# Kernel optimization log

Hardware: AMD Instinct MI355X
Metric: run time of the kernel (lower is better)

The kernel has to match this reference:

```python
import jax, jax.numpy as jnp
import numpy as np

C = 1.0
TAU = 1.0
LE = 1.0
LH = 1.0
LN_EPS = 1e-5

def _safe_norm(x, keepdims=False):
    return jnp.clip(jnp.sqrt(jnp.sum(x * x, axis=-1, keepdims=keepdims)), 1e-15)

def _project_to_ball(x, c, eps=1e-5):
    sqrt_c = c ** 0.5
    norm = _safe_norm(x, keepdims=True)
    max_norm = (1.0 - eps) / sqrt_c
    scale = jnp.where(norm > max_norm, max_norm / norm, 1.0)
    return x * scale

def _lambda_x(x, c):
    x = _project_to_ball(x, c)
    x2 = jnp.sum(x * x, axis=-1, keepdims=True)
    return 2.0 / jnp.clip(1.0 - c * x2, 1e-15)

def _mobius_add(x, y, c):
    x = _project_to_ball(x, c)
    y = _project_to_ball(y, c)
    x2 = jnp.sum(x * x, axis=-1, keepdims=True)
    y2 = jnp.sum(y * y, axis=-1, keepdims=True)
    xy = jnp.sum(x * y, axis=-1, keepdims=True)
    num = (1 + 2 * c * xy + c * y2) * x + (1 - c * x2) * y
    den = 1 + 2 * c * xy + c ** 2 * x2 * y2
    return num / jnp.clip(den, 1e-15)

def _exp_map_x(x, v, c):
    sqrt_c = c ** 0.5
    lam = _lambda_x(x, c)
    vnorm = _safe_norm(v, keepdims=True)
    v_dir = v / vnorm
    factor = jnp.tanh(lam * sqrt_c * vnorm / 2.0) / sqrt_c
    out = _mobius_add(x, v_dir * factor, c)
    return _project_to_ball(out, c)

def _log_map_x(x, y, c):
    sqrt_c = c ** 0.5
    lam = _lambda_x(x, c)
    u = _mobius_add(-x, y, c)
    unorm = _safe_norm(u, keepdims=True)
    u_dir = u / unorm
    arg = jnp.minimum(sqrt_c * unorm, 1 - 1e-7)
    scale = 2.0 / (lam * sqrt_c) * jnp.arctanh(arg)
    return scale * u_dir

def _poincare_distance_sq(x, y, c):
    sqrt_c = c ** 0.5
    x = _project_to_ball(x, c)
    y = _project_to_ball(y, c)
    diff = _mobius_add(-x, y, c)
    norm = _safe_norm(diff, keepdims=False)
    arg = jnp.minimum(sqrt_c * norm, 1 - 1e-7)
    dist = 2.0 / sqrt_c * jnp.arctanh(arg)
    return dist * dist

def setup_inputs() -> dict:
    key = jax.random.key(0)
    ks = jax.random.split(key, 6)
    B, N, L, A, de, dh, z_dim = 8, 8, 64, 64, 128, 64, 128
    z_e, z_h = z_dim // 2 + z_dim % 2, z_dim // 2
    return {
        "curr_rho_batch": jax.random.normal(ks[0], (B, A, de), jnp.float32),
        "curr_hyp_emb": 0.1 * jax.random.normal(ks[1], (B, dh), jnp.float32),
        "demo_rho_batch": jax.random.normal(ks[2], (B, N, L, A, de), jnp.float32),
        "demo_hyp_emb": 0.1 * jax.random.normal(ks[3], (B, N, L, dh), jnp.float32),
        "We": 0.02 * jax.random.normal(ks[4], (z_e, de), jnp.float32),
        "Wh": 0.02 * jax.random.normal(ks[5], (z_h, dh), jnp.float32),
        "ln_gamma": jnp.ones((z_dim,), jnp.float32),
        "ln_beta": jnp.zeros((z_dim,), jnp.float32),
    }

def reference(curr_rho_batch, curr_hyp_emb, demo_rho_batch, demo_hyp_emb, We, Wh, ln_gamma, ln_beta):
    B, A, de = curr_rho_batch.shape
    _, N, L, _, _ = demo_rho_batch.shape
    M = N * L
    dh = curr_hyp_emb.shape[-1]
    demo_rho_flat = demo_rho_batch.reshape(B, M, A, de)   # [B,M,A,de]
    demo_hyp_flat = demo_hyp_emb.reshape(B, M, dh)        # [B,M,dh]
    # Euclidean squared distances: [B,M,A] -> [B,A,M]
    e_diff_sq = jnp.sum((curr_rho_batch[:, None, :, :] - demo_rho_flat) ** 2, axis=-1)
    e_diff_sq = jnp.transpose(e_diff_sq, (0, 2, 1))
    # Hyperbolic squared distances: [B,M]
    dH2 = _poincare_distance_sq(curr_hyp_emb[:, None, :], demo_hyp_flat, C)
    scores = -(LH * dH2[:, None, :] + LE * e_diff_sq) / max(TAU, 1e-8)  # [B,A,M]
    alpha = jax.nn.softmax(scores, axis=-1)
    # Euclidean aggregation
    e_out = jnp.einsum('bam,bmad->bad', alpha, demo_rho_flat)  # [B,A,de]
    # Hyperbolic Karcher-mean step
    log_vecs = _log_map_x(curr_hyp_emb[:, None, :], demo_hyp_flat, C)  # [B,M,dh]
    v = jnp.einsum('bam,bmd->bad', alpha, log_vecs)  # [B,A,dh]
    x_ba = jnp.broadcast_to(curr_hyp_emb[:, None, :], (B, A, dh))
    h_out = _exp_map_x(x_ba, v, C)  # [B,A,dh]
    z = jnp.concatenate([e_out @ We.T, h_out @ Wh.T], axis=-1)  # [B,A,z_dim]
    mean = jnp.mean(z, axis=-1, keepdims=True)
    var = jnp.var(z, axis=-1, keepdims=True)
    z = (z - mean) / jnp.sqrt(var + LN_EPS) * ln_gamma + ln_beta
    return z
```

## Files before the change

### kernel.cpp

```cpp
#include <hip/hip_runtime.h>

#define DEV __device__ __forceinline__

constexpr int A_ = 64, DE = 128, M_ = 512, DH = 64;

DEV float wred_sum64(float v) {
#pragma unroll
    for (int o = 1; o < 64; o <<= 1) v += __shfl_xor(v, o, 64);
    return v;
}

__global__ __launch_bounds__(256) void k_hyp(const float* __restrict__ curr_hyp,
                                             const float* __restrict__ demo_hyp,
                                             float* __restrict__ dH2,
                                             float* __restrict__ logv) {
    const int lane = threadIdx.x & 63;
    const int r    = (blockIdx.x << 2) + (threadIdx.x >> 6);
    const int b    = r >> 9;

    float x = curr_hyp[(b << 6) + lane];
    float y = demo_hyp[((size_t)r << 6) + lane];
    const float mx = 1.0f - 1e-5f;

    float x2r = wred_sum64(x * x);
    float xn  = fmaxf(sqrtf(x2r), 1e-15f);
    float sx  = xn > mx ? mx / xn : 1.0f;
    x *= sx;
    float x2 = x2r * sx * sx;
    float y2r = wred_sum64(y * y);
    float yn  = fmaxf(sqrtf(y2r), 1e-15f);
    float sy  = yn > mx ? mx / yn : 1.0f;
    y *= sy;
    float y2 = y2r * sy * sy;

    float xy = wred_sum64(x * y);
    float num = (1.f - 2.f * xy + y2) * (-x) + (1.f - x2) * y;
    float den = fmaxf(1.f - 2.f * xy + x2 * y2, 1e-15f);
    float u   = num / den;

    float u2  = wred_sum64(u * u);
    float un  = fmaxf(sqrtf(u2), 1e-15f);
    float arg = fminf(un, 1.f - 1e-7f);
    float at  = 0.5f * __logf((1.f + arg) / (1.f - arg));

    if (lane == 0) dH2[r] = 4.f * at * at;

    float lamden = fmaxf(1.f - x2, 1e-15f);
    float ls     = lamden * at / un;
    logv[((size_t)r << 6) + lane] = ls * u;
}

__global__ __launch_bounds__(512, 4) void k_main(const float* __restrict__ curr_rho,
                                                 const float* __restrict__ demo_rho,
                                                 const float* __restrict__ curr_hyp,
                                                 const float* __restrict__ dH2,
                                                 const float* __restrict__ logv,
                                                 const float* __restrict__ We,
                                                 const float* __restrict__ Wh,
                                                 const float* __restrict__ gamma,
                                                 const float* __restrict__ beta,
                                                 float* __restrict__ out) {
    __shared__ __align__(16) float rede[32 * 132];
    __shared__ float lds_sc[512];
    __shared__ float lds_dh[512];
    __shared__ float redm[8];
    __shared__ float reds[8];
    __shared__ float vpart[8][64];
    __shared__ float eh[192];

    const int t    = threadIdx.x;
    const int lane = t & 63;
    const int wv   = t >> 6;
    const int dp   = t & 15;
    const int mi   = t >> 4;
    const int blk  = blockIdx.x;
    const int b    = blk >> 6, a = blk & 63;

    lds_dh[t] = dH2[(b << 9) + t];

    float qf[8];
    {
        float4 q0 = *(const float4*)(curr_rho + (size_t)blk * DE + dp * 8);
        float4 q1 = *(const float4*)(curr_rho + (size_t)blk * DE + dp * 8 + 4);
        qf[0] = q0.x; qf[1] = q0.y; qf[2] = q0.z; qf[3] = q0.w;
        qf[4] = q1.x; qf[5] = q1.y; qf[6] = q1.z; qf[7] = q1.w;
    }

    const size_t rowStride = (size_t)A_ * DE;
    const size_t cstep     = (size_t)32 * rowStride;
    const float* tp = demo_rho + ((size_t)b * M_ * A_ + a) * DE + (size_t)mi * rowStride + dp * 8;

    __syncthreads();

    float4 ka0 = *(const float4*)tp;
    float4 ka1 = *(const float4*)(tp + 4);
    float4 kb0 = *(const float4*)(tp + cstep);
    float4 kb1 = *(const float4*)(tp + cstep + 4);

    float e_acc[8];
#pragma unroll
    for (int j = 0; j < 8; j++) e_acc[j] = 0.f;
    float gmax = -1e30f, gsum = 0.f;

#pragma unroll 2
    for (int c = 0; c < 16; ++c) {
        float4 n0, n1;
        if (c + 2 < 16) {
            const float* np = tp + (size_t)(c + 2) * cstep;
            n0 = *(const float4*)np;
            n1 = *(const float4*)(np + 4);
        }
        float kf[8];
        kf[0] = ka0.x; kf[1] = ka0.y; kf[2] = ka0.z; kf[3] = ka0.w;
        kf[4] = ka1.x; kf[5] = ka1.y; kf[6] = ka1.z; kf[7] = ka1.w;

        float ps = 0.f;
#pragma unroll
        for (int j = 0; j < 8; j++) { float d = qf[j] - kf[j]; ps += d * d; }
        ps += __shfl_xor(ps, 1, 64);
        ps += __shfl_xor(ps, 2, 64);
        ps += __shfl_xor(ps, 4, 64);
        ps += __shfl_xor(ps, 8, 64);
        float sc = -(lds_dh[c * 32 + mi] + ps);
        if (dp == 0) lds_sc[c * 32 + mi] = sc;

        float lm = fmaxf(sc, __shfl_xor(sc, 16, 64));
        lm = fmaxf(lm, __shfl_xor(lm, 32, 64));
        float gnew = fmaxf(gmax, lm);
        float r1   = __expf(gmax - gnew);
        float wexp = __expf(sc - gnew);
        float wsum = wexp + __shfl_xor(wexp, 16, 64);
        wsum += __shfl_xor(wsum, 32, 64);
        gsum = fmaf(gsum, r1, wsum);
#pragma unroll
        for (int j = 0; j < 8; j++) e_acc[j] = fmaf(wexp, kf[j], e_acc[j] * r1);
        gmax = gnew;

        ka0 = kb0; ka1 = kb1; kb0 = n0; kb1 = n1;
    }

    if (lane == 0) { redm[wv] = gmax; reds[wv] = gsum; }
    __syncthreads();

    float M = redm[0];
#pragma unroll
    for (int w = 1; w < 8; w++) M = fmaxf(M, redm[w]);
    float S = 0.f;
#pragma unroll
    for (int w = 0; w < 8; w++) S += reds[w] * __expf(redm[w] - M);
    const float inv = 1.f / S;
    const float fw  = __expf(gmax - M);

    float al = __expf(lds_sc[t] - M) * inv;

    *(float4*)&rede[mi * 132 + dp * 8] =
        make_float4(e_acc[0] * fw, e_acc[1] * fw, e_acc[2] * fw, e_acc[3] * fw);
    *(float4*)&rede[mi * 132 + dp * 8 + 4] =
        make_float4(e_acc[4] * fw, e_acc[5] * fw, e_acc[6] * fw, e_acc[7] * fw);
    lds_sc[t] = al;
    __syncthreads();

    if (t < 128) {
        float s = 0.f;
#pragma unroll
        for (int g = 0; g < 32; g++) s += rede[g * 132 + t];
        eh[t] = s * inv;
    }

    {
        const float* lvb = logv + ((size_t)(b * M_) + wv * 64) * DH;
        float acc = 0.f;
#pragma unroll 8
        for (int i = 0; i < 64; ++i)
            acc = fmaf(lds_sc[wv * 64 + i], lvb[(size_t)i * DH + lane], acc);
        vpart[wv][lane] = acc;
    }
    __syncthreads();

    if (wv == 0) {
        float v = 0.f;
#pragma unroll
        for (int w = 0; w < 8; w++) v += vpart[w][lane];

        const float mx = 1.0f - 1e-5f;
        float x = curr_hyp[(b << 6) + lane];
        float x2r = wred_sum64(x * x);
        float xn  = fmaxf(sqrtf(x2r), 1e-15f);
        float sx  = xn > mx ? mx / xn : 1.f;
        x *= sx;
        float x2 = x2r * sx * sx;
        float lamden = fmaxf(1.f - x2, 1e-15f);

        float v2 = wred_sum64(v * v);
        float vn = fmaxf(sqrtf(v2), 1e-15f);
        float targ   = vn / lamden;
        float e2     = __expf(2.f * targ);
        float factor = 1.f - 2.f / (e2 + 1.f);
        float wvv    = v * (factor / vn);

        float w2 = wred_sum64(wvv * wvv);
        float xw = wred_sum64(x * wvv);
        float num = (1.f + 2.f * xw + w2) * x + (1.f - x2) * wvv;
        float den = fmaxf(1.f + 2.f * xw + x2 * w2, 1e-15f);
        float h   = num / den;
        float h2  = wred_sum64(h * h);
        float hn  = fmaxf(sqrtf(h2), 1e-15f);
        float shh = hn > mx ? mx / hn : 1.f;
        h *= shh;
        eh[128 + lane] = h;

        float ze = 0.f;
        const float* werow = We + lane * 128;
#pragma unroll
        for (int d0 = 0; d0 < 128; d0 += 4) {
            float4 wv4 = *(const float4*)(werow + d0);
            ze = fmaf(eh[d0 + 0], wv4.x, ze);
            ze = fmaf(eh[d0 + 1], wv4.y, ze);
            ze = fmaf(eh[d0 + 2], wv4.z, ze);
            ze = fmaf(eh[d0 + 3], wv4.w, ze);
        }
        float zh = 0.f;
        const float* whrow = Wh + lane * 64;
#pragma unroll
        for (int d0 = 0; d0 < 64; d0 += 4) {
            float4 wv4 = *(const float4*)(whrow + d0);
            zh = fmaf(eh[128 + d0 + 0], wv4.x, zh);
            zh = fmaf(eh[128 + d0 + 1], wv4.y, zh);
            zh = fmaf(eh[128 + d0 + 2], wv4.z, zh);
            zh = fmaf(eh[128 + d0 + 3], wv4.w, zh);
        }
        float ssum = wred_sum64(ze + zh);
        float mean = ssum * (1.f / 128.f);
        float sq   = wred_sum64(ze * ze + zh * zh);
        float var  = sq * (1.f / 128.f) - mean * mean;
        float rinv = rsqrtf(var + 1e-5f);
        float oe = (ze - mean) * rinv * gamma[lane] + beta[lane];
        float oh = (zh - mean) * rinv * gamma[64 + lane] + beta[64 + lane];
        out[(size_t)blk * 128 + lane]      = oe;
        out[(size_t)blk * 128 + 64 + lane] = oh;
    }
}

extern "C" void kernel_launch(void* const* d_in, const int* in_sizes, int n_in,
                              void* d_out, int out_size, void* d_ws, size_t ws_size,
                              hipStream_t stream) {
    const float* curr_rho = (const float*)d_in[0];
    const float* curr_hyp = (const float*)d_in[1];
    const float* demo_rho = (const float*)d_in[2];
    const float* demo_hyp = (const float*)d_in[3];
    const float* We       = (const float*)d_in[4];
    const float* Wh       = (const float*)d_in[5];
    const float* gamma    = (const float*)d_in[6];
    const float* beta     = (const float*)d_in[7];
    float* out = (float*)d_out;

    float* ws   = (float*)d_ws;
    float* dH2  = ws;
    float* logv = ws + 4096;

    k_hyp<<<1024, 256, 0, stream>>>(curr_hyp, demo_hyp, dH2, logv);
    k_main<<<512, 512, 0, stream>>>(curr_rho, demo_rho, curr_hyp, dH2, logv,
                                    We, Wh, gamma, beta, out);
}
```

Baseline: 209.9 us.

## Split main kernel into split-M online-softmax stream pass and combine kernel

Replaces the single per-(b,a) main kernel with a flash-decoding style split: k_stream processes 16-row chunks of M per block with an online softmax, streaming demo_rho with register prefetch, and writes partial max/sum/accumulators and raw scores to workspace. k_comb merges the 32 partials per (b,a), recomputes the hyperbolic weighted sum from the stored scores, and applies the exp map, projections and layernorm. The aim is to read the large demo_rho tensor with better parallelism and coalescing. The cost is an extra launch and several MB of workspace traffic. The old kernel is kept as a fallback when the workspace is too small.

```diff
diff --git a/kernel.cpp b/kernel.cpp
--- a/kernel.cpp
+++ b/kernel.cpp
@@ -50,16 +50,237 @@
     logv[((size_t)r << 6) + lane] = ls * u;
 }
 
-__global__ __launch_bounds__(512, 4) void k_main(const float* __restrict__ curr_rho,
+__global__ __launch_bounds__(1024) void k_stream(const float* __restrict__ curr_rho,
                                                  const float* __restrict__ demo_rho,
-                                                 const float* __restrict__ curr_hyp,
                                                  const float* __restrict__ dH2,
-                                                 const float* __restrict__ logv,
-                                                 const float* __restrict__ We,
-                                                 const float* __restrict__ Wh,
-                                                 const float* __restrict__ gamma,
-                                                 const float* __restrict__ beta,
-                                                 float* __restrict__ out) {
+                                                 float* __restrict__ ws_m,
+                                                 float* __restrict__ ws_s,
+                                                 float* __restrict__ ws_e,
+                                                 float* __restrict__ ws_sc) {
+    const int t   = threadIdx.x;
+    const int mi  = t >> 4;
+    const int dp  = t & 15;
+    const int blk = blockIdx.x;
+    const int b   = blk >> 5, mc = blk & 31;
+    const int m0  = mc << 4;
+
+    float qf[8];
+    {
+        const float* qp = curr_rho + ((size_t)(b * 64 + mi)) * DE + dp * 8;
+        float4 q0 = *(const float4*)qp;
+        float4 q1 = *(const float4*)(qp + 4);
+        qf[0] = q0.x; qf[1] = q0.y; qf[2] = q0.z; qf[3] = q0.w;
+        qf[4] = q1.x; qf[5] = q1.y; qf[6] = q1.z; qf[7] = q1.w;
+    }
+
+    float dh2r[16];
+    {
+        const float* dp2 = dH2 + (b << 9) + m0;
+        *(float4*)&dh2r[0]  = *(const float4*)(dp2);
+        *(float4*)&dh2r[4]  = *(const float4*)(dp2 + 4);
+        *(float4*)&dh2r[8]  = *(const float4*)(dp2 + 8);
+        *(float4*)&dh2r[12] = *(const float4*)(dp2 + 12);
+    }
+
+    const float* tp = demo_rho + ((size_t)(b * M_ + m0)) * (A_ * DE) + mi * DE + dp * 8;
+
+    float4 pa0 = *(const float4*)tp;
+    float4 pa1 = *(const float4*)(tp + 4);
+    float4 pb0 = *(const float4*)(tp + 8192);
+    float4 pb1 = *(const float4*)(tp + 8192 + 4);
+    float4 pc0 = *(const float4*)(tp + 16384);
+    float4 pc1 = *(const float4*)(tp + 16384 + 4);
+
+    float e_acc[8];
+#pragma unroll
+    for (int j = 0; j < 8; j++) e_acc[j] = 0.f;
+    float gmax = -1e30f, gsum = 0.f;
+
+    float* scp = ws_sc + ((size_t)blk * 16) * 64;
+
+#pragma unroll
+    for (int c = 0; c < 16; ++c) {
+        float4 n0 = make_float4(0.f, 0.f, 0.f, 0.f);
+        float4 n1 = n0;
+        if (c + 3 < 16) {
+            const float* np = tp + (size_t)(c + 3) * 8192;
+            n0 = *(const float4*)np;
+            n1 = *(const float4*)(np + 4);
+        }
+        float kf[8];
+        kf[0] = pa0.x; kf[1] = pa0.y; kf[2] = pa0.z; kf[3] = pa0.w;
+        kf[4] = pa1.x; kf[5] = pa1.y; kf[6] = pa1.z; kf[7] = pa1.w;
+
+        float ps = 0.f;
+#pragma unroll
+        for (int j = 0; j < 8; j++) { float d = qf[j] - kf[j]; ps += d * d; }
+        ps += __shfl_xor(ps, 1, 64);
+        ps += __shfl_xor(ps, 2, 64);
+        ps += __shfl_xor(ps, 4, 64);
+        ps += __shfl_xor(ps, 8, 64);
+
+        float sc = -(dh2r[c] + ps);
+        if (dp == 0) scp[c * 64 + mi] = sc;
+
+        float gnew = fmaxf(gmax, sc);
+        float r1   = __expf(gmax - gnew);
+        float w    = __expf(sc - gnew);
+        gsum = fmaf(gsum, r1, w);
+#pragma unroll
+        for (int j = 0; j < 8; j++) e_acc[j] = fmaf(w, kf[j], e_acc[j] * r1);
+        gmax = gnew;
+
+        pa0 = pb0; pa1 = pb1; pb0 = pc0; pb1 = pc1; pc0 = n0; pc1 = n1;
+    }
+
+    float* ep = ws_e + ((size_t)(blk * 64 + mi)) * 128 + dp * 8;
+    *(float4*)ep       = make_float4(e_acc[0], e_acc[1], e_acc[2], e_acc[3]);
+    *(float4*)(ep + 4) = make_float4(e_acc[4], e_acc[5], e_acc[6], e_acc[7]);
+    if (dp == 0) {
+        ws_m[blk * 64 + mi] = gmax;
+        ws_s[blk * 64 + mi] = gsum;
+    }
+}
+
+__global__ __launch_bounds__(256) void k_comb(const float* __restrict__ curr_hyp,
+                                              const float* __restrict__ logv,
+                                              const float* __restrict__ ws_m,
+                                              const float* __restrict__ ws_s,
+                                              const float* __restrict__ ws_e,
+                                              const float* __restrict__ ws_sc,
+                                              const float* __restrict__ We,
+                                              const float* __restrict__ Wh,
+                                              const float* __restrict__ gamma,
+                                              const float* __restrict__ beta,
+                                              float* __restrict__ out) {
+    __shared__ float facL[32];
+    __shared__ float sMS[2];
+    __shared__ float ehL[192];
+    __shared__ float vpart[4][64];
+
+    const int t   = threadIdx.x;
+    const int blk = blockIdx.x;
+    const int b   = blk >> 6, a = blk & 63;
+
+    float g = -1e30f, s = 0.f;
+    if (t < 32) {
+        g = ws_m[(size_t)(b * 32 + t) * 64 + a];
+        s = ws_s[(size_t)(b * 32 + t) * 64 + a];
+    }
+    float M = g;
+    M = fmaxf(M, __shfl_xor(M, 1, 64));
+    M = fmaxf(M, __shfl_xor(M, 2, 64));
+    M = fmaxf(M, __shfl_xor(M, 4, 64));
+    M = fmaxf(M, __shfl_xor(M, 8, 64));
+    M = fmaxf(M, __shfl_xor(M, 16, 64));
+    float fac = __expf(g - M);
+    float Sp  = s * fac;
+    Sp += __shfl_xor(Sp, 1, 64);
+    Sp += __shfl_xor(Sp, 2, 64);
+    Sp += __shfl_xor(Sp, 4, 64);
+    Sp += __shfl_xor(Sp, 8, 64);
+    Sp += __shfl_xor(Sp, 16, 64);
+    if (t < 32) facL[t] = fac;
+    if (t == 0) { sMS[0] = M; sMS[1] = Sp; }
+    __syncthreads();
+    const float Mg   = sMS[0];
+    const float invS = 1.f / sMS[1];
+
+    if (t < 128) {
+        float acc = 0.f;
+#pragma unroll
+        for (int mc = 0; mc < 32; ++mc)
+            acc = fmaf(ws_e[((size_t)((b * 32 + mc) * 64 + a)) * 128 + t], facL[mc], acc);
+        ehL[t] = acc * invS;
+    }
+
+    {
+        const int dh = t & 63, sg = t >> 6;
+        const float* lvb = logv  + ((size_t)(b * M_ + sg * 128)) * 64 + dh;
+        const float* scb = ws_sc + ((size_t)(b * M_ + sg * 128)) * 64 + a;
+        float vac = 0.f;
+#pragma unroll 8
+        for (int i = 0; i < 128; ++i) {
+            float w = __expf(scb[(size_t)i * 64] - Mg);
+            vac = fmaf(w, lvb[(size_t)i * 64], vac);
+        }
+        vpart[sg][dh] = vac;
+    }
+    __syncthreads();
+
+    if (t < 64) {
+        const int lane = t;
+        float v = (vpart[0][lane] + vpart[1][lane] + vpart[2][lane] + vpart[3][lane]) * invS;
+
+        const float mx = 1.0f - 1e-5f;
+        float x = curr_hyp[(b << 6) + lane];
+        float x2r = wred_sum64(x * x);
+        float xn  = fmaxf(sqrtf(x2r), 1e-15f);
+        float sx  = xn > mx ? mx / xn : 1.f;
+        x *= sx;
+        float x2 = x2r * sx * sx;
+        float lamden = fmaxf(1.f - x2, 1e-15f);
+
+        float v2 = wred_sum64(v * v);
+        float vn = fmaxf(sqrtf(v2), 1e-15f);
+        float targ   = vn / lamden;
+        float e2     = __expf(2.f * targ);
+        float factor = 1.f - 2.f / (e2 + 1.f);
+        float wvv    = v * (factor / vn);
+
+        float w2 = wred_sum64(wvv * wvv);
+        float xw = wred_sum64(x * wvv);
+        float num = (1.f + 2.f * xw + w2) * x + (1.f - x2) * wvv;
+        float den = fmaxf(1.f + 2.f * xw + x2 * w2, 1e-15f);
+        float h   = num / den;
+        float h2  = wred_sum64(h * h);
+        float hn  = fmaxf(sqrtf(h2), 1e-15f);
+        float shh = hn > mx ? mx / hn : 1.f;
+        h *= shh;
+        ehL[128 + lane] = h;
+
+        float ze = 0.f;
+        const float* werow = We + lane * 128;
+#pragma unroll
+        for (int d0 = 0; d0 < 128; d0 += 4) {
+            float4 wv4 = *(const float4*)(werow + d0);
+            ze = fmaf(ehL[d0 + 0], wv4.x, ze);
+            ze = fmaf(ehL[d0 + 1], wv4.y, ze);
+            ze = fmaf(ehL[d0 + 2], wv4.z, ze);
+            ze = fmaf(ehL[d0 + 3], wv4.w, ze);
+        }
+        float zh = 0.f;
+        const float* whrow = Wh + lane * 64;
+#pragma unroll
+        for (int d0 = 0; d0 < 64; d0 += 4) {
+            float4 wv4 = *(const float4*)(whrow + d0);
+            zh = fmaf(ehL[128 + d0 + 0], wv4.x, zh);
+            zh = fmaf(ehL[128 + d0 + 1], wv4.y, zh);
+            zh = fmaf(ehL[128 + d0 + 2], wv4.z, zh);
+            zh = fmaf(ehL[128 + d0 + 3], wv4.w, zh);
+        }
+        float ssum = wred_sum64(ze + zh);
+        float mean = ssum * (1.f / 128.f);
+        float sq   = wred_sum64(ze * ze + zh * zh);
+        float var  = sq * (1.f / 128.f) - mean * mean;
+        float rinv = rsqrtf(var + 1e-5f);
+        float oe = (ze - mean) * rinv * gamma[lane] + beta[lane];
+        float oh = (zh - mean) * rinv * gamma[64 + lane] + beta[64 + lane];
+        out[(size_t)blk * 128 + lane]      = oe;
+        out[(size_t)blk * 128 + 64 + lane] = oh;
+    }
+}
+
+__global__ __launch_bounds__(512, 4) void k_main_fb(const float* __restrict__ curr_rho,
+                                                    const float* __restrict__ demo_rho,
+                                                    const float* __restrict__ curr_hyp,
+                                                    const float* __restrict__ dH2,
+                                                    const float* __restrict__ logv,
+                                                    const float* __restrict__ We,
+                                                    const float* __restrict__ Wh,
+                                                    const float* __restrict__ gamma,
+                                                    const float* __restrict__ beta,
+                                                    float* __restrict__ out) {
     __shared__ __align__(16) float rede[32 * 132];
     __shared__ float lds_sc[512];
     __shared__ float lds_dh[512];
@@ -259,6 +480,18 @@
     float* logv = ws + 4096;
 
     k_hyp<<<1024, 256, 0, stream>>>(curr_hyp, demo_hyp, dH2, logv);
-    k_main<<<512, 512, 0, stream>>>(curr_rho, demo_rho, curr_hyp, dH2, logv,
-                                    We, Wh, gamma, beta, out);
-}
+
+    const size_t NEED = (size_t)2658304 * sizeof(float);
+    if (ws_size >= NEED) {
+        float* ws_m  = ws + 266240;
+        float* ws_s  = ws + 282624;
+        float* ws_e  = ws + 299008;
+        float* ws_sc = ws + 2396160;
+        k_stream<<<256, 1024, 0, stream>>>(curr_rho, demo_rho, dH2, ws_m, ws_s, ws_e, ws_sc);
+        k_comb<<<512, 256, 0, stream>>>(curr_hyp, logv, ws_m, ws_s, ws_e, ws_sc,
+                                        We, Wh, gamma, beta, out);
+    } else {
+        k_main_fb<<<512, 512, 0, stream>>>(curr_rho, demo_rho, curr_hyp, dH2, logv,
+                                           We, Wh, gamma, beta, out);
+    }
+}
```

After: 240.4 us. +14.5%, slower.

## Split attention into split-M streaming kernel and separate combine kernel

Applied to the files above, without the earlier changes.

Restructures the main kernel so each block covers 4 agents over a quarter of the demo slots. Each wave reads contiguous 2KB rows of demo_rho instead of strided 512B rows, and prefetch depth goes from 2 to 3. Partial max, sum, weighted e-sums and raw scores are written to the workspace. A new combine kernel merges the four partials, recomputes the softmax weights from the stored scores, and runs the hyperbolic aggregation, exp map, projection and layernorm. This adds one kernel launch and extra global traffic for scores and partials in exchange for better coalescing of the dominant demo_rho stream.

```diff
diff --git a/kernel.cpp b/kernel.cpp
--- a/kernel.cpp
+++ b/kernel.cpp
@@ -50,69 +50,72 @@
     logv[((size_t)r << 6) + lane] = ls * u;
 }
 
-__global__ __launch_bounds__(512, 4) void k_main(const float* __restrict__ curr_rho,
-                                                 const float* __restrict__ demo_rho,
-                                                 const float* __restrict__ curr_hyp,
-                                                 const float* __restrict__ dH2,
-                                                 const float* __restrict__ logv,
-                                                 const float* __restrict__ We,
-                                                 const float* __restrict__ Wh,
-                                                 const float* __restrict__ gamma,
-                                                 const float* __restrict__ beta,
-                                                 float* __restrict__ out) {
-    __shared__ __align__(16) float rede[32 * 132];
-    __shared__ float lds_sc[512];
-    __shared__ float lds_dh[512];
-    __shared__ float redm[8];
-    __shared__ float reds[8];
-    __shared__ float vpart[8][64];
-    __shared__ float eh[192];
-
-    const int t    = threadIdx.x;
-    const int lane = t & 63;
-    const int wv   = t >> 6;
-    const int dp   = t & 15;
-    const int mi   = t >> 4;
-    const int blk  = blockIdx.x;
-    const int b    = blk >> 6, a = blk & 63;
-
-    lds_dh[t] = dH2[(b << 9) + t];
+__global__ __launch_bounds__(512, 4) void k_stream2(const float* __restrict__ curr_rho,
+                                                    const float* __restrict__ demo_rho,
+                                                    const float* __restrict__ dH2,
+                                                    float* __restrict__ ws_m,
+                                                    float* __restrict__ ws_s,
+                                                    float* __restrict__ ws_e,
+                                                    float* __restrict__ ws_sc) {
+    __shared__ float lds_dh[128];
+    __shared__ float redm[8][4];
+    __shared__ float reds[8][4];
+    __shared__ __align__(16) float rede[8][512];
+
+    const int t  = threadIdx.x;
+    const int l  = t & 63;
+    const int mi = t >> 6;
+    const int al = l >> 4;
+    const int dp = l & 15;
+    const int blk = blockIdx.x;
+    const int b  = blk >> 6;
+    const int rr = blk & 63;
+    const int mq = rr >> 4;
+    const int aq = rr & 15;
+    const int a  = aq * 4 + al;
+    const int m0 = mq << 7;
+
+    if (t < 128) lds_dh[t] = dH2[(b << 9) + m0 + t];
 
     float qf[8];
     {
-        float4 q0 = *(const float4*)(curr_rho + (size_t)blk * DE + dp * 8);
-        float4 q1 = *(const float4*)(curr_rho + (size_t)blk * DE + dp * 8 + 4);
+        const float* qp = curr_rho + ((size_t)(b * 64 + a)) * DE + dp * 8;
+        float4 q0 = *(const float4*)qp;
+        float4 q1 = *(const float4*)(qp + 4);
         qf[0] = q0.x; qf[1] = q0.y; qf[2] = q0.z; qf[3] = q0.w;
         qf[4] = q1.x; qf[5] = q1.y; qf[6] = q1.z; qf[7] = q1.w;
     }
 
-    const size_t rowStride = (size_t)A_ * DE;
-    const size_t cstep     = (size_t)32 * rowStride;
-    const float* tp = demo_rho + ((size_t)b * M_ * A_ + a) * DE + (size_t)mi * rowStride + dp * 8;
+    const float* tp = demo_rho + ((size_t)(b * M_ + m0)) * (A_ * DE)
+                    + (size_t)mi * 8192 + aq * 4 * DE + al * DE + dp * 8;
+    const size_t CS = 65536;
 
     __syncthreads();
 
-    float4 ka0 = *(const float4*)tp;
-    float4 ka1 = *(const float4*)(tp + 4);
-    float4 kb0 = *(const float4*)(tp + cstep);
-    float4 kb1 = *(const float4*)(tp + cstep + 4);
+    float4 pa0 = *(const float4*)tp;
+    float4 pa1 = *(const float4*)(tp + 4);
+    float4 pb0 = *(const float4*)(tp + CS);
+    float4 pb1 = *(const float4*)(tp + CS + 4);
+    float4 pc0 = *(const float4*)(tp + 2 * CS);
+    float4 pc1 = *(const float4*)(tp + 2 * CS + 4);
 
     float e_acc[8];
 #pragma unroll
     for (int j = 0; j < 8; j++) e_acc[j] = 0.f;
     float gmax = -1e30f, gsum = 0.f;
 
-#pragma unroll 2
+#pragma unroll 4
     for (int c = 0; c < 16; ++c) {
-        float4 n0, n1;
-        if (c + 2 < 16) {
-            const float* np = tp + (size_t)(c + 2) * cstep;
+        float4 n0 = make_float4(0.f, 0.f, 0.f, 0.f);
+        float4 n1 = n0;
+        if (c + 3 < 16) {
+            const float* np = tp + (size_t)(c + 3) * CS;
             n0 = *(const float4*)np;
             n1 = *(const float4*)(np + 4);
         }
         float kf[8];
-        kf[0] = ka0.x; kf[1] = ka0.y; kf[2] = ka0.z; kf[3] = ka0.w;
-        kf[4] = ka1.x; kf[5] = ka1.y; kf[6] = ka1.z; kf[7] = ka1.w;
+        kf[0] = pa0.x; kf[1] = pa0.y; kf[2] = pa0.z; kf[3] = pa0.w;
+        kf[4] = pa1.x; kf[5] = pa1.y; kf[6] = pa1.z; kf[7] = pa1.w;
 
         float ps = 0.f;
 #pragma unroll
@@ -121,66 +124,108 @@
         ps += __shfl_xor(ps, 2, 64);
         ps += __shfl_xor(ps, 4, 64);
         ps += __shfl_xor(ps, 8, 64);
-        float sc = -(lds_dh[c * 32 + mi] + ps);
-        if (dp == 0) lds_sc[c * 32 + mi] = sc;
-
-        float lm = fmaxf(sc, __shfl_xor(sc, 16, 64));
-        lm = fmaxf(lm, __shfl_xor(lm, 32, 64));
-        float gnew = fmaxf(gmax, lm);
+
+        float sc = -(lds_dh[c * 8 + mi] + ps);
+        if (dp == 0)
+            ws_sc[((size_t)(b * M_ + m0 + c * 8 + mi)) * 64 + a] = sc;
+
+        float gnew = fmaxf(gmax, sc);
         float r1   = __expf(gmax - gnew);
-        float wexp = __expf(sc - gnew);
-        float wsum = wexp + __shfl_xor(wexp, 16, 64);
-        wsum += __shfl_xor(wsum, 32, 64);
-        gsum = fmaf(gsum, r1, wsum);
-#pragma unroll
-        for (int j = 0; j < 8; j++) e_acc[j] = fmaf(wexp, kf[j], e_acc[j] * r1);
+        float w    = __expf(sc - gnew);
+        gsum = fmaf(gsum, r1, w);
+#pragma unroll
+        for (int j = 0; j < 8; j++) e_acc[j] = fmaf(w, kf[j], e_acc[j] * r1);
         gmax = gnew;
 
-        ka0 = kb0; ka1 = kb1; kb0 = n0; kb1 = n1;
-    }
-
-    if (lane == 0) { redm[wv] = gmax; reds[wv] = gsum; }
+        pa0 = pb0; pa1 = pb1; pb0 = pc0; pb1 = pc1; pc0 = n0; pc1 = n1;
+    }
+
+    if (dp == 0) { redm[mi][al] = gmax; reds[mi][al] = gsum; }
     __syncthreads();
 
-    float M = redm[0];
-#pragma unroll
-    for (int w = 1; w < 8; w++) M = fmaxf(M, redm[w]);
+    float Mb = redm[0][al];
+#pragma unroll
+    for (int k = 1; k < 8; k++) Mb = fmaxf(Mb, redm[k][al]);
+    float Sb = 0.f;
+#pragma unroll
+    for (int k = 0; k < 8; k++) Sb += reds[k][al] * __expf(redm[k][al] - Mb);
+    float fac = __expf(gmax - Mb);
+
+    *(float4*)&rede[mi][al * 128 + dp * 8] =
+        make_float4(e_acc[0] * fac, e_acc[1] * fac, e_acc[2] * fac, e_acc[3] * fac);
+    *(float4*)&rede[mi][al * 128 + dp * 8 + 4] =
+        make_float4(e_acc[4] * fac, e_acc[5] * fac, e_acc[6] * fac, e_acc[7] * fac);
+    if (mi == 0 && dp == 0) {
+        const int q = b * 4 + mq;
+        ws_m[q * 64 + a] = Mb;
+        ws_s[q * 64 + a] = Sb;
+    }
+    __syncthreads();
+
+    {
+        const int al2 = t >> 7, dd = t & 127;
+        float s = 0.f;
+#pragma unroll
+        for (int k = 0; k < 8; k++) s += rede[k][al2 * 128 + dd];
+        ws_e[((size_t)(b * 4 + mq) * 64 + (aq * 4 + al2)) * 128 + dd] = s;
+    }
+}
+
+__global__ __launch_bounds__(256) void k_comb2(const float* __restrict__ curr_hyp,
+                                               const float* __restrict__ logv,
+                                               const float* __restrict__ ws_m,
+                                               const float* __restrict__ ws_s,
+                                               const float* __restrict__ ws_e,
+                                               const float* __restrict__ ws_sc,
+                                               const float* __restrict__ We,
+                                               const float* __restrict__ Wh,
+                                               const float* __restrict__ gamma,
+                                               const float* __restrict__ beta,
+                                               float* __restrict__ out) {
+    __shared__ float ehL[192];
+    __shared__ float vpart[4][64];
+
+    const int t   = threadIdx.x;
+    const int blk = blockIdx.x;
+    const int b   = blk >> 6, a = blk & 63;
+
+    float m_[4], s_[4];
+#pragma unroll
+    for (int q = 0; q < 4; q++) {
+        m_[q] = ws_m[(b * 4 + q) * 64 + a];
+        s_[q] = ws_s[(b * 4 + q) * 64 + a];
+    }
+    float M = fmaxf(fmaxf(m_[0], m_[1]), fmaxf(m_[2], m_[3]));
     float S = 0.f;
 #pragma unroll
-    for (int w = 0; w < 8; w++) S += reds[w] * __expf(redm[w] - M);
-    const float inv = 1.f / S;
-    const float fw  = __expf(gmax - M);
-
-    float al = __expf(lds_sc[t] - M) * inv;
-
-    *(float4*)&rede[mi * 132 + dp * 8] =
-        make_float4(e_acc[0] * fw, e_acc[1] * fw, e_acc[2] * fw, e_acc[3] * fw);
-    *(float4*)&rede[mi * 132 + dp * 8 + 4] =
-        make_float4(e_acc[4] * fw, e_acc[5] * fw, e_acc[6] * fw, e_acc[7] * fw);
-    lds_sc[t] = al;
+    for (int q = 0; q < 4; q++) S += s_[q] * __expf(m_[q] - M);
+    const float invS = 1.f / S;
+
+    if (t < 128) {
+        float acc = 0.f;
+#pragma unroll
+        for (int q = 0; q < 4; q++)
+            acc = fmaf(ws_e[((size_t)(b * 4 + q) * 64 + a) * 128 + t], __expf(m_[q] - M), acc);
+        ehL[t] = acc * invS;
+    }
+
+    {
+        const int dh = t & 63, sg = t >> 6;
+        const float* lvb = logv  + ((size_t)(b * M_ + sg * 128)) * 64 + dh;
+        const float* scb = ws_sc + ((size_t)(b * M_ + sg * 128)) * 64 + a;
+        float vac = 0.f;
+#pragma unroll 8
+        for (int i = 0; i < 128; ++i) {
+            float w = __expf(scb[(size_t)i * 64] - M);
+            vac = fmaf(w, lvb[(size_t)i * 64], vac);
+        }
+        vpart[sg][dh] = vac;
+    }
     __syncthreads();
 
-    if (t < 128) {
-        float s = 0.f;
-#pragma unroll
-        for (int g = 0; g < 32; g++) s += rede[g * 132 + t];
-        eh[t] = s * inv;
-    }
-
-    {
-        const float* lvb = logv + ((size_t)(b * M_) + wv * 64) * DH;
-        float acc = 0.f;
-#pragma unroll 8
-        for (int i = 0; i < 64; ++i)
-            acc = fmaf(lds_sc[wv * 64 + i], lvb[(size_t)i * DH + lane], acc);
-        vpart[wv][lane] = acc;
-    }
-    __syncthreads();
-
-    if (wv == 0) {
-        float v = 0.f;
-#pragma unroll
-        for (int w = 0; w < 8; w++) v += vpart[w][lane];
+    if (t < 64) {
+        const int lane = t;
+        float v = (vpart[0][lane] + vpart[1][lane] + vpart[2][lane] + vpart[3][lane]) * invS;
 
         const float mx = 1.0f - 1e-5f;
         float x = curr_hyp[(b << 6) + lane];
@@ -207,27 +252,27 @@
         float hn  = fmaxf(sqrtf(h2), 1e-15f);
         float shh = hn > mx ? mx / hn : 1.f;
         h *= shh;
-        eh[128 + lane] = h;
+        ehL[128 + lane] = h;
 
         float ze = 0.f;
         const float* werow = We + lane * 128;
 #pragma unroll
         for (int d0 = 0; d0 < 128; d0 += 4) {
             float4 wv4 = *(const float4*)(werow + d0);
-            ze = fmaf(eh[d0 + 0], wv4.x, ze);
-            ze = fmaf(eh[d0 + 1], wv4.y, ze);
-            ze = fmaf(eh[d0 + 2], wv4.z, ze);
-            ze = fmaf(eh[d0 + 3], wv4.w, ze);
+            ze = fmaf(ehL[d0 + 0], wv4.x, ze);
+            ze = fmaf(ehL[d0 + 1], wv4.y, ze);
+            ze = fmaf(ehL[d0 + 2], wv4.z, ze);
+            ze = fmaf(ehL[d0 + 3], wv4.w, ze);
         }
         float zh = 0.f;
         const float* whrow = Wh + lane * 64;
 #pragma unroll
         for (int d0 = 0; d0 < 64; d0 += 4) {
             float4 wv4 = *(const float4*)(whrow + d0);
-            zh = fmaf(eh[128 + d0 + 0], wv4.x, zh);
-            zh = fmaf(eh[128 + d0 + 1], wv4.y, zh);
-            zh = fmaf(eh[128 + d0 + 2], wv4.z, zh);
-            zh = fmaf(eh[128 + d0 + 3], wv4.w, zh);
+            zh = fmaf(ehL[128 + d0 + 0], wv4.x, zh);
+            zh = fmaf(ehL[128 + d0 + 1], wv4.y, zh);
+            zh = fmaf(ehL[128 + d0 + 2], wv4.z, zh);
+            zh = fmaf(ehL[128 + d0 + 3], wv4.w, zh);
         }
         float ssum = wred_sum64(ze + zh);
         float mean = ssum * (1.f / 128.f);
@@ -254,11 +299,16 @@
     const float* beta     = (const float*)d_in[7];
     float* out = (float*)d_out;
 
-    float* ws   = (float*)d_ws;
-    float* dH2  = ws;
-    float* logv = ws + 4096;
+    float* ws    = (float*)d_ws;
+    float* dH2   = ws;
+    float* logv  = ws + 4096;
+    float* ws_m  = ws + 266240;
+    float* ws_s  = ws + 268288;
+    float* ws_e  = ws + 270336;
+    float* ws_sc = ws + 532480;
 
     k_hyp<<<1024, 256, 0, stream>>>(curr_hyp, demo_hyp, dH2, logv);
-    k_main<<<512, 512, 0, stream>>>(curr_rho, demo_rho, curr_hyp, dH2, logv,
-                                    We, Wh, gamma, beta, out);
-}
+    k_stream2<<<512, 512, 0, stream>>>(curr_rho, demo_rho, dH2, ws_m, ws_s, ws_e, ws_sc);
+    k_comb2<<<512, 256, 0, stream>>>(curr_hyp, logv, ws_m, ws_s, ws_e, ws_sc,
+                                     We, Wh, gamma, beta, out);
+}
```

After: 221.6 us. +5.6%, slower.

## Split attention over M into two halves with separate combine kernel

Applied to the files above, without the earlier changes.

The main kernel is split into a partial kernel that processes half of the 512 demo rows per block (1024 blocks instead of 512), writing partial max, sum, weighted Euclidean accumulators and raw scores to workspace. A new combine kernel merges the two halves with log-sum-exp rescaling, recomputes the softmax weights, does the hyperbolic aggregation, exp-map, projections and layernorm. This is meant to give the streaming of demo_rho more parallelism across the GPU's compute units, at the cost of an extra launch and workspace round trips.

```diff
diff --git a/kernel.cpp b/kernel.cpp
--- a/kernel.cpp
+++ b/kernel.cpp
@@ -50,23 +50,17 @@
     logv[((size_t)r << 6) + lane] = ls * u;
 }
 
-__global__ __launch_bounds__(512, 4) void k_main(const float* __restrict__ curr_rho,
-                                                 const float* __restrict__ demo_rho,
-                                                 const float* __restrict__ curr_hyp,
-                                                 const float* __restrict__ dH2,
-                                                 const float* __restrict__ logv,
-                                                 const float* __restrict__ We,
-                                                 const float* __restrict__ Wh,
-                                                 const float* __restrict__ gamma,
-                                                 const float* __restrict__ beta,
-                                                 float* __restrict__ out) {
-    __shared__ __align__(16) float rede[32 * 132];
-    __shared__ float lds_sc[512];
-    __shared__ float lds_dh[512];
+__global__ __launch_bounds__(512, 8) void k_ms(const float* __restrict__ curr_rho,
+                                               const float* __restrict__ demo_rho,
+                                               const float* __restrict__ dH2,
+                                               float* __restrict__ ws_m,
+                                               float* __restrict__ ws_s,
+                                               float* __restrict__ ws_e,
+                                               float* __restrict__ ws_sc) {
+    __shared__ float lds_dh[256];
     __shared__ float redm[8];
     __shared__ float reds[8];
-    __shared__ float vpart[8][64];
-    __shared__ float eh[192];
+    __shared__ __align__(16) float rede[32 * 132];
 
     const int t    = threadIdx.x;
     const int lane = t & 63;
@@ -74,21 +68,25 @@
     const int dp   = t & 15;
     const int mi   = t >> 4;
     const int blk  = blockIdx.x;
-    const int b    = blk >> 6, a = blk & 63;
-
-    lds_dh[t] = dH2[(b << 9) + t];
+    const int h    = blk & 1;
+    const int ba   = blk >> 1;
+    const int b    = ba >> 6, a = ba & 63;
+
+    if (t < 256) lds_dh[t] = dH2[(b << 9) + (h << 8) + t];
 
     float qf[8];
     {
-        float4 q0 = *(const float4*)(curr_rho + (size_t)blk * DE + dp * 8);
-        float4 q1 = *(const float4*)(curr_rho + (size_t)blk * DE + dp * 8 + 4);
+        const float* qp = curr_rho + (size_t)ba * DE + dp * 8;
+        float4 q0 = *(const float4*)qp;
+        float4 q1 = *(const float4*)(qp + 4);
         qf[0] = q0.x; qf[1] = q0.y; qf[2] = q0.z; qf[3] = q0.w;
         qf[4] = q1.x; qf[5] = q1.y; qf[6] = q1.z; qf[7] = q1.w;
     }
 
     const size_t rowStride = (size_t)A_ * DE;
     const size_t cstep     = (size_t)32 * rowStride;
-    const float* tp = demo_rho + ((size_t)b * M_ * A_ + a) * DE + (size_t)mi * rowStride + dp * 8;
+    const float* tp = demo_rho + ((size_t)(b * M_ + h * 256) * A_ + a) * DE
+                    + (size_t)mi * rowStride + dp * 8;
 
     __syncthreads();
 
@@ -103,9 +101,9 @@
     float gmax = -1e30f, gsum = 0.f;
 
 #pragma unroll 2
-    for (int c = 0; c < 16; ++c) {
+    for (int c = 0; c < 8; ++c) {
         float4 n0, n1;
-        if (c + 2 < 16) {
+        if (c + 2 < 8) {
             const float* np = tp + (size_t)(c + 2) * cstep;
             n0 = *(const float4*)np;
             n1 = *(const float4*)(np + 4);
@@ -122,7 +120,8 @@
         ps += __shfl_xor(ps, 4, 64);
         ps += __shfl_xor(ps, 8, 64);
         float sc = -(lds_dh[c * 32 + mi] + ps);
-        if (dp == 0) lds_sc[c * 32 + mi] = sc;
+        if (dp == 0)
+            ws_sc[(size_t)ba * M_ + h * 256 + c * 32 + mi] = sc;
 
         float lm = fmaxf(sc, __shfl_xor(sc, 16, 64));
         lm = fmaxf(lm, __shfl_xor(lm, 32, 64));
@@ -142,45 +141,80 @@
     if (lane == 0) { redm[wv] = gmax; reds[wv] = gsum; }
     __syncthreads();
 
-    float M = redm[0];
-#pragma unroll
-    for (int w = 1; w < 8; w++) M = fmaxf(M, redm[w]);
-    float S = 0.f;
-#pragma unroll
-    for (int w = 0; w < 8; w++) S += reds[w] * __expf(redm[w] - M);
-    const float inv = 1.f / S;
-    const float fw  = __expf(gmax - M);
-
-    float al = __expf(lds_sc[t] - M) * inv;
+    float Mb = redm[0];
+#pragma unroll
+    for (int w = 1; w < 8; w++) Mb = fmaxf(Mb, redm[w]);
+    float Sb = 0.f;
+#pragma unroll
+    for (int w = 0; w < 8; w++) Sb += reds[w] * __expf(redm[w] - Mb);
+    const float fac = __expf(gmax - Mb);
 
     *(float4*)&rede[mi * 132 + dp * 8] =
-        make_float4(e_acc[0] * fw, e_acc[1] * fw, e_acc[2] * fw, e_acc[3] * fw);
+        make_float4(e_acc[0] * fac, e_acc[1] * fac, e_acc[2] * fac, e_acc[3] * fac);
     *(float4*)&rede[mi * 132 + dp * 8 + 4] =
-        make_float4(e_acc[4] * fw, e_acc[5] * fw, e_acc[6] * fw, e_acc[7] * fw);
-    lds_sc[t] = al;
+        make_float4(e_acc[4] * fac, e_acc[5] * fac, e_acc[6] * fac, e_acc[7] * fac);
+    if (t == 0) { ws_m[blk] = Mb; ws_s[blk] = Sb; }
     __syncthreads();
 
     if (t < 128) {
         float s = 0.f;
 #pragma unroll
         for (int g = 0; g < 32; g++) s += rede[g * 132 + t];
-        eh[t] = s * inv;
+        ws_e[(size_t)blk * 128 + t] = s;
+    }
+}
+
+__global__ __launch_bounds__(256) void k_comb_s(const float* __restrict__ curr_hyp,
+                                                const float* __restrict__ logv,
+                                                const float* __restrict__ ws_m,
+                                                const float* __restrict__ ws_s,
+                                                const float* __restrict__ ws_e,
+                                                const float* __restrict__ ws_sc,
+                                                const float* __restrict__ We,
+                                                const float* __restrict__ Wh,
+                                                const float* __restrict__ gamma,
+                                                const float* __restrict__ beta,
+                                                float* __restrict__ out) {
+    __shared__ float wL[512];
+    __shared__ float ehL[192];
+    __shared__ float vpart[4][64];
+
+    const int t   = threadIdx.x;
+    const int blk = blockIdx.x;
+    const int b   = blk >> 6, a = blk & 63;
+    const size_t ba = (size_t)blk;
+
+    const float m0 = ws_m[ba * 2], m1 = ws_m[ba * 2 + 1];
+    const float s0 = ws_s[ba * 2], s1 = ws_s[ba * 2 + 1];
+    const float M  = fmaxf(m0, m1);
+    const float f0 = __expf(m0 - M), f1 = __expf(m1 - M);
+    const float invS = 1.f / (s0 * f0 + s1 * f1);
+
+    if (t < 128) {
+        float acc = ws_e[ba * 256 + t] * f0 + ws_e[ba * 256 + 128 + t] * f1;
+        ehL[t] = acc * invS;
     }
 
     {
-        const float* lvb = logv + ((size_t)(b * M_) + wv * 64) * DH;
-        float acc = 0.f;
+        float2 scv = ((const float2*)(ws_sc + ba * 512))[t];
+        wL[2 * t]     = __expf(scv.x - M);
+        wL[2 * t + 1] = __expf(scv.y - M);
+    }
+
+    {
+        const int dh = t & 63, sg = t >> 6;
+        const float* lvb = logv + ((size_t)(b * M_ + sg * 128)) * 64 + dh;
+        float vac = 0.f;
 #pragma unroll 8
-        for (int i = 0; i < 64; ++i)
-            acc = fmaf(lds_sc[wv * 64 + i], lvb[(size_t)i * DH + lane], acc);
-        vpart[wv][lane] = acc;
+        for (int i = 0; i < 128; ++i)
+            vac = fmaf(wL[sg * 128 + i], lvb[(size_t)i * 64], vac);
+        vpart[sg][dh] = vac;
     }
     __syncthreads();
 
-    if (wv == 0) {
-        float v = 0.f;
-#pragma unroll
-        for (int w = 0; w < 8; w++) v += vpart[w][lane];
+    if (t < 64) {
+        const int lane = t;
+        float v = (vpart[0][lane] + vpart[1][lane] + vpart[2][lane] + vpart[3][lane]) * invS;
 
         const float mx = 1.0f - 1e-5f;
         float x = curr_hyp[(b << 6) + lane];
@@ -202,32 +236,32 @@
         float xw = wred_sum64(x * wvv);
         float num = (1.f + 2.f * xw + w2) * x + (1.f - x2) * wvv;
         float den = fmaxf(1.f + 2.f * xw + x2 * w2, 1e-15f);
-        float h   = num / den;
-        float h2  = wred_sum64(h * h);
+        float hh  = num / den;
+        float h2  = wred_sum64(hh * hh);
         float hn  = fmaxf(sqrtf(h2), 1e-15f);
         float shh = hn > mx ? mx / hn : 1.f;
-        h *= shh;
-        eh[128 + lane] = h;
+        hh *= shh;
+        ehL[128 + lane] = hh;
 
         float ze = 0.f;
         const float* werow = We + lane * 128;
 #pragma unroll
         for (int d0 = 0; d0 < 128; d0 += 4) {
             float4 wv4 = *(const float4*)(werow + d0);
-            ze = fmaf(eh[d0 + 0], wv4.x, ze);
-            ze = fmaf(eh[d0 + 1], wv4.y, ze);
-            ze = fmaf(eh[d0 + 2], wv4.z, ze);
-            ze = fmaf(eh[d0 + 3], wv4.w, ze);
+            ze = fmaf(ehL[d0 + 0], wv4.x, ze);
+            ze = fmaf(ehL[d0 + 1], wv4.y, ze);
+            ze = fmaf(ehL[d0 + 2], wv4.z, ze);
+            ze = fmaf(ehL[d0 + 3], wv4.w, ze);
         }
         float zh = 0.f;
         const float* whrow = Wh + lane * 64;
 #pragma unroll
         for (int d0 = 0; d0 < 64; d0 += 4) {
             float4 wv4 = *(const float4*)(whrow + d0);
-            zh = fmaf(eh[128 + d0 + 0], wv4.x, zh);
-            zh = fmaf(eh[128 + d0 + 1], wv4.y, zh);
-            zh = fmaf(eh[128 + d0 + 2], wv4.z, zh);
-            zh = fmaf(eh[128 + d0 + 3], wv4.w, zh);
+            zh = fmaf(ehL[128 + d0 + 0], wv4.x, zh);
+            zh = fmaf(ehL[128 + d0 + 1], wv4.y, zh);
+            zh = fmaf(ehL[128 + d0 + 2], wv4.z, zh);
+            zh = fmaf(ehL[128 + d0 + 3], wv4.w, zh);
         }
         float ssum = wred_sum64(ze + zh);
         float mean = ssum * (1.f / 128.f);
@@ -254,11 +288,16 @@
     const float* beta     = (const float*)d_in[7];
     float* out = (float*)d_out;
 
-    float* ws   = (float*)d_ws;
-    float* dH2  = ws;
-    float* logv = ws + 4096;
+    float* ws    = (float*)d_ws;
+    float* dH2   = ws;
+    float* logv  = ws + 4096;
+    float* ws_m  = ws + 266240;
+    float* ws_s  = ws + 267264;
+    float* ws_e  = ws + 268288;
+    float* ws_sc = ws + 399360;
 
     k_hyp<<<1024, 256, 0, stream>>>(curr_hyp, demo_hyp, dH2, logv);
-    k_main<<<512, 512, 0, stream>>>(curr_rho, demo_rho, curr_hyp, dH2, logv,
-                                    We, Wh, gamma, beta, out);
-}
+    k_ms<<<1024, 512, 0, stream>>>(curr_rho, demo_rho, dH2, ws_m, ws_s, ws_e, ws_sc);
+    k_comb_s<<<512, 256, 0, stream>>>(curr_hyp, logv, ws_m, ws_s, ws_e, ws_sc,
+                                      We, Wh, gamma, beta, out);
+}
```

Measured after the change: 224.7 us. 1.07x slower.
